# Kernel tuning notes

Hardware: AMD Instinct MI355X
Metric: run time of the kernel (lower is better)

Reference implementation:

```python
import jax, jax.numpy as jnp
import numpy as np

BN_EPS = 1e-5


def setup_inputs() -> dict:
    key = jax.random.key(0)
    ks = jax.random.split(key, 7)
    B, C, N = 8, 512, 2048
    P = C // 2
    x = jax.random.normal(ks[0], (B, C, N), dtype=jnp.float32)
    # 1x1 conv weights (no bias), shape [out, in]
    Wg = jax.random.normal(ks[1], (P, C), dtype=jnp.float32) * (1.0 / np.sqrt(C))
    Wtheta = jax.random.normal(ks[2], (P, C), dtype=jnp.float32) * (1.0 / np.sqrt(C))
    Wphi = jax.random.normal(ks[3], (P, C), dtype=jnp.float32) * (1.0 / np.sqrt(C))
    Wz = jax.random.normal(ks[4], (C, P), dtype=jnp.float32) * (1.0 / np.sqrt(P))
    gamma = jnp.ones((C,), dtype=jnp.float32)
    beta = jnp.zeros((C,), dtype=jnp.float32)
    return {"x": x, "Wg": Wg, "Wtheta": Wtheta, "Wphi": Wphi, "Wz": Wz,
            "gamma": gamma, "beta": beta}


def reference(x, Wg, Wtheta, Wphi, Wz, gamma, beta):
    # x: [B, C, N]
    g = jnp.einsum('pc,bcn->bnp', Wg, x)        # [B, N, P]
    theta = jnp.einsum('pc,bcn->bnp', Wtheta, x)  # [B, N, P]
    phi = jnp.einsum('pc,bcn->bpn', Wphi, x)      # [B, P, N]
    f = jnp.einsum('bnp,bpm->bnm', theta, phi)    # [B, N, N] unscaled scores
    f = jax.nn.softmax(f, axis=-1)
    y = jnp.einsum('bnm,bmp->bpn', f, g)          # [B, P, N]
    z = jnp.einsum('cp,bpn->bcn', Wz, y)          # [B, C, N]
    # BatchNorm1d (training-mode batch stats over batch and length dims)
    mean = jnp.mean(z, axis=(0, 2), keepdims=True)
    var = jnp.mean((z - mean) ** 2, axis=(0, 2), keepdims=True)
    z_bn = (z - mean) / jnp.sqrt(var + BN_EPS)
    z_bn = z_bn * gamma[None, :, None] + beta[None, :, None]
    return z_bn + x
```

## Files before the change

kernel.cpp:

```cpp
#include <hip/hip_runtime.h>
#include <hip/hip_bf16.h>


typedef __attribute__((ext_vector_type(8))) short short8;
typedef __attribute__((ext_vector_type(4))) float floatx4;

__device__ __forceinline__ unsigned short f2bf(float v) {
    __hip_bfloat16 h = __float2bfloat16(v);
    return *(unsigned short*)&h;
}
__device__ __forceinline__ float bf2f(unsigned short u) {
    __hip_bfloat16 h;
    *(unsigned short*)&h = u;
    return __bfloat162float(h);
}

__global__ __launch_bounds__(256) void transpose_split(
    const float* __restrict__ X, unsigned short* __restrict__ Thi,
    unsigned short* __restrict__ Tlo, int R, int N)
{
    X   += (long)blockIdx.z * R * N;
    Thi += (long)blockIdx.z * N * R;
    Tlo += (long)blockIdx.z * N * R;
    __shared__ float s[32][33];
    const int tx = threadIdx.x & 31, ty = threadIdx.x >> 5;
    const int n0 = blockIdx.x * 32, r0 = blockIdx.y * 32;
#pragma unroll
    for (int r = 0; r < 4; ++r)
        s[ty + r * 8][tx] = X[(long)(r0 + ty + r * 8) * N + n0 + tx];
    __syncthreads();
#pragma unroll
    for (int r = 0; r < 4; ++r) {
        const int n = ty + r * 8;
        const float v = s[tx][n];
        const unsigned short hi = f2bf(v);
        const unsigned short lo = f2bf(v - bf2f(hi));
        Thi[(long)(n0 + n) * R + r0 + tx] = hi;
        Tlo[(long)(n0 + n) * R + r0 + tx] = lo;
    }
}

__global__ __launch_bounds__(256) void split_w2(
    const float* __restrict__ Wth, const float* __restrict__ Wph,
    unsigned short* __restrict__ Whi, unsigned short* __restrict__ Wlo, int PC)
{
    const int i = blockIdx.x * 256 + threadIdx.x;
    if (i < 2 * PC) {
        const float v = (i < PC) ? Wth[i] : Wph[i - PC];
        const unsigned short hi = f2bf(v);
        Whi[i] = hi;
        Wlo[i] = f2bf(v - bf2f(hi));
    }
}

__global__ __launch_bounds__(256) void cast_bf16(
    const float* __restrict__ X, unsigned short* __restrict__ Y)
{
    const long i = ((long)blockIdx.x * 256 + threadIdx.x) * 4;
    const float4 v = *(const float4*)&X[i];
    ushort4 o;
    o.x = f2bf(v.x); o.y = f2bf(v.y); o.z = f2bf(v.z); o.w = f2bf(v.w);
    *(ushort4*)&Y[i] = o;
}

#define BK 32

template <bool SPLIT, int OUTMODE, int FM, int FN>
__global__ __launch_bounds__(256) void mfma_gemm(
    const unsigned short* __restrict__ Ahi, const unsigned short* __restrict__ Alo,
    const unsigned short* __restrict__ Bhi, const unsigned short* __restrict__ Blo,
    void* __restrict__ Cout, void* __restrict__ Cout2,
    int K, int lda, int ldb, int ldc,
    long sA, long sB, long sC,
    float* __restrict__ S1, float* __restrict__ S2)
{
    constexpr int MTM = FM * 32, MTN = FN * 32;
    constexpr int SA = FM / 2, SB = FN / 2;

    Ahi += (long)blockIdx.z * sA;
    Bhi += (long)blockIdx.z * sB;
    if (SPLIT) { Alo += (long)blockIdx.z * sA; Blo += (long)blockIdx.z * sB; }
    float* Cf = (float*)Cout + (long)blockIdx.z * sC;
    unsigned short* Ch = (unsigned short*)Cout + (long)blockIdx.z * sC;
    unsigned short* Cl = (unsigned short*)Cout2 + (long)blockIdx.z * sC;

    __shared__ unsigned short AsH[MTM * BK], BsH[MTN * BK];
    __shared__ unsigned short AsL[SPLIT ? MTM * BK : 8], BsL[SPLIT ? MTN * BK : 8];

    const int tid = threadIdx.x;
    const int wid = tid >> 6, lane = tid & 63;
    const int wm = (wid >> 1) * (FM * 16), wn = (wid & 1) * (FN * 16);
    const int l15 = lane & 15, quad = lane >> 4;
    const int m0 = blockIdx.y * MTM, n0 = blockIdx.x * MTN;

    int arow[SA], acol[SA], brow[SB], bcol[SB];
#pragma unroll
    for (int t = 0; t < SA; ++t) {
        const int gid = t * 256 + tid;
        arow[t] = gid >> 2; acol[t] = (gid & 3) * 8;
    }
#pragma unroll
    for (int t = 0; t < SB; ++t) {
        const int gid = t * 256 + tid;
        brow[t] = gid >> 2; bcol[t] = (gid & 3) * 8;
    }

    short8 pa[SA], pb[SB], paL[SPLIT ? SA : 1], pbL[SPLIT ? SB : 1];

    auto loadTiles = [&](int k0) {
#pragma unroll
        for (int t = 0; t < SA; ++t) {
            const long o = (long)(m0 + arow[t]) * lda + k0 + acol[t];
            pa[t] = *(const short8*)&Ahi[o];
            if (SPLIT) paL[t] = *(const short8*)&Alo[o];
        }
#pragma unroll
        for (int t = 0; t < SB; ++t) {
            const long o = (long)(n0 + brow[t]) * ldb + k0 + bcol[t];
            pb[t] = *(const short8*)&Bhi[o];
            if (SPLIT) pbL[t] = *(const short8*)&Blo[o];
        }
    };
    auto writeTiles = [&]() {
#pragma unroll
        for (int t = 0; t < SA; ++t) {
            *(short8*)&AsH[arow[t] * BK + acol[t]] = pa[t];
            if (SPLIT) *(short8*)&AsL[arow[t] * BK + acol[t]] = paL[t];
        }
#pragma unroll
        for (int t = 0; t < SB; ++t) {
            *(short8*)&BsH[brow[t] * BK + bcol[t]] = pb[t];
            if (SPLIT) *(short8*)&BsL[brow[t] * BK + bcol[t]] = pbL[t];
        }
    };

    floatx4 acc[FM][FN];
#pragma unroll
    for (int i = 0; i < FM; ++i)
#pragma unroll
        for (int j = 0; j < FN; ++j) acc[i][j] = (floatx4){0.f, 0.f, 0.f, 0.f};

    const int iters = K / BK;
    loadTiles(0);
    writeTiles();
    __syncthreads();

    for (int it = 0; it < iters; ++it) {
        if (it + 1 < iters) loadTiles((it + 1) * BK);

        short8 ah[FM], bh[FN], al[SPLIT ? FM : 1], bl[SPLIT ? FN : 1];
#pragma unroll
        for (int i = 0; i < FM; ++i) {
            ah[i] = *(const short8*)&AsH[(wm + i * 16 + l15) * BK + quad * 8];
            if (SPLIT) al[i] = *(const short8*)&AsL[(wm + i * 16 + l15) * BK + quad * 8];
        }
#pragma unroll
        for (int j = 0; j < FN; ++j) {
            bh[j] = *(const short8*)&BsH[(wn + j * 16 + l15) * BK + quad * 8];
            if (SPLIT) bl[j] = *(const short8*)&BsL[(wn + j * 16 + l15) * BK + quad * 8];
        }
#pragma unroll
        for (int i = 0; i < FM; ++i)
#pragma unroll
            for (int j = 0; j < FN; ++j) {
                acc[i][j] = __builtin_amdgcn_mfma_f32_16x16x32_bf16(ah[i], bh[j], acc[i][j], 0, 0, 0);
                if (SPLIT) {
                    acc[i][j] = __builtin_amdgcn_mfma_f32_16x16x32_bf16(ah[i], bl[j], acc[i][j], 0, 0, 0);
                    acc[i][j] = __builtin_amdgcn_mfma_f32_16x16x32_bf16(al[i], bh[j], acc[i][j], 0, 0, 0);
                }
            }

        if (it + 1 < iters) {
            __syncthreads();
            writeTiles();
            __syncthreads();
        }
    }

#pragma unroll
    for (int i = 0; i < FM; ++i)
#pragma unroll
        for (int j = 0; j < FN; ++j) {
            const int m = m0 + wm + i * 16 + quad * 4;
            const int n = n0 + wn + j * 16 + l15;
#pragma unroll
            for (int r = 0; r < 4; ++r) {
                const float v = acc[i][j][r];
                const long idx = (long)(m + r) * ldc + n;
                if (OUTMODE == 0) {
                    Cf[idx] = v;
                } else if (OUTMODE == 1 || OUTMODE == 3) {
                    Ch[idx] = f2bf(v);
                } else {
                    const unsigned short hi = f2bf(v);
                    Ch[idx] = hi;
                    Cl[idx] = f2bf(v - bf2f(hi));
                }
            }
        }

    if (OUTMODE == 3) {
        const int slot = (blockIdx.z * gridDim.x + blockIdx.x) * 2 + (wn >> 6);
#pragma unroll
        for (int i = 0; i < FM; ++i)
#pragma unroll
            for (int r = 0; r < 4; ++r) {
                float s = 0.f, q = 0.f;
#pragma unroll
                for (int j = 0; j < FN; ++j) {
                    const float v = acc[i][j][r];
                    s += v; q += v * v;
                }
#pragma unroll
                for (int msk = 1; msk < 16; msk <<= 1) {
                    s += __shfl_xor(s, msk, 64);
                    q += __shfl_xor(q, msk, 64);
                }
                if (l15 == 0) {
                    const int row = m0 + wm + i * 16 + quad * 4 + r;
                    S1[(long)row * 256 + slot] = s;
                    S2[(long)row * 256 + slot] = q;
                }
            }
    }
}

#define PSTRP 136

__device__ __forceinline__ int swz64(int row, int slot) {
    return (row << 6) + (((slot ^ row) & 7) << 3);
}

__global__ __launch_bounds__(256, 2) void fused_attn(
    const unsigned short* __restrict__ thphH,
    const unsigned short* __restrict__ thphL,
    const unsigned short* __restrict__ gbf,
    float* __restrict__ yp,
    float2* __restrict__ ml)
{
    const int N = 2048, P = 256, P2 = 512;
    const int id = blockIdx.x;
    const int b  = id & 7;
    const int kh = (id >> 3) & 3;
    const int qt = id >> 5;
    const int q0 = qt * 64;

    const unsigned short* thB = thphH + (long)b * N * P2;
    const unsigned short* tlB = thphL + (long)b * N * P2;
    const unsigned short* gB  = gbf   + (long)b * P * N;
    float*  ypB = yp + (long)kh * (8L * N * P) + (long)b * N * P;
    float2* mlB = ml + (long)kh * (8L * N) + (long)b * N;

    __shared__ unsigned short FG[2 * 128 * 64];
    unsigned short* Fh = FG;
    unsigned short* Fl = FG + 128 * 64;
    unsigned short* Gs = FG;
    __shared__ unsigned short Pw[4][16 * PSTRP];
    __shared__ float Aly[64];

    const int tid = threadIdx.x;
    const int wid = tid >> 6, lane = tid & 63;
    const int l15 = lane & 15, quad = lane >> 4;

    short8 tHr[8], tLr[8];
    {
        const unsigned short* t1 = thB + (long)(q0 + wid * 16 + l15) * P2;
        const unsigned short* t2 = tlB + (long)(q0 + wid * 16 + l15) * P2;
#pragma unroll
        for (int kt = 0; kt < 8; ++kt) {
            tHr[kt] = *(const short8*)&t1[kt * 32 + quad * 8];
            tLr[kt] = *(const short8*)&t2[kt * 32 + quad * 8];
        }
    }

    float mrun[4], lrun[4];
#pragma unroll
    for (int r = 0; r < 4; ++r) { mrun[r] = -1e30f; lrun[r] = 0.f; }

    floatx4 oacc[16];
#pragma unroll
    for (int p = 0; p < 16; ++p) oacc[p] = (floatx4){0.f, 0.f, 0.f, 0.f};

    const int prow = tid >> 3, slot = tid & 7;
    short8 pfH[4], pfL[4], pg[8];

    auto loadPhi = [&](int m0, int kc) {
#pragma unroll
        for (int s = 0; s < 4; ++s) {
            const long o = (long)(m0 + prow + s * 32) * P2 + P + kc * 64 + slot * 8;
            pfH[s] = *(const short8*)&thB[o];
            pfL[s] = *(const short8*)&tlB[o];
        }
    };
    auto writePhi = [&]() {
#pragma unroll
        for (int s = 0; s < 4; ++s) {
            *(short8*)&Fh[swz64(prow + s * 32, slot)] = pfH[s];
            *(short8*)&Fl[swz64(prow + s * 32, slot)] = pfL[s];
        }
    };
    auto loadG = [&](int m0, int mc) {
#pragma unroll
        for (int s = 0; s < 8; ++s)
            pg[s] = *(const short8*)&gB[(long)(prow + s * 32) * N + m0 + mc * 64 + slot * 8];
    };
    auto writeG = [&]() {
#pragma unroll
        for (int s = 0; s < 8; ++s)
            *(short8*)&Gs[swz64(prow + s * 32, slot)] = pg[s];
    };

    for (int mt = 0; mt < 4; ++mt) {
        const int m0 = kh * 512 + mt * 128;

        floatx4 sacc[8];
#pragma unroll
        for (int j = 0; j < 8; ++j) sacc[j] = (floatx4){0.f, 0.f, 0.f, 0.f};

        loadPhi(m0, 0);
        __syncthreads();
        writePhi();
        __syncthreads();
#pragma unroll
        for (int kc = 0; kc < 4; ++kc) {
            if (kc < 3) loadPhi(m0, kc + 1);
#pragma unroll
            for (int ks = 0; ks < 2; ++ks) {
                const short8 aH = tHr[kc * 2 + ks];
                const short8 aL = tLr[kc * 2 + ks];
#pragma unroll
                for (int j = 0; j < 8; ++j) {
                    const int ro = swz64(j * 16 + l15, ks * 4 + quad);
                    const short8 bh = *(const short8*)&Fh[ro];
                    const short8 bl = *(const short8*)&Fl[ro];
                    sacc[j] = __builtin_amdgcn_mfma_f32_16x16x32_bf16(aH, bh, sacc[j], 0, 0, 0);
                    sacc[j] = __builtin_amdgcn_mfma_f32_16x16x32_bf16(aH, bl, sacc[j], 0, 0, 0);
                    sacc[j] = __builtin_amdgcn_mfma_f32_16x16x32_bf16(aL, bh, sacc[j], 0, 0, 0);
                }
            }
            if (kc < 3) {
                __syncthreads();
                writePhi();
                __syncthreads();
            }
        }

        float alpha[4];
#pragma unroll
        for (int r = 0; r < 4; ++r) {
            float v = sacc[0][r];
#pragma unroll
            for (int j = 1; j < 8; ++j) v = fmaxf(v, sacc[j][r]);
            v = fmaxf(v, __shfl_xor(v, 1, 64));
            v = fmaxf(v, __shfl_xor(v, 2, 64));
            v = fmaxf(v, __shfl_xor(v, 4, 64));
            v = fmaxf(v, __shfl_xor(v, 8, 64));
            const float mo = mrun[r];
            const float mn = fmaxf(mo, v);
            mrun[r] = mn;
            alpha[r] = __expf(mo - mn);
        }
        float lpart[4] = {0.f, 0.f, 0.f, 0.f};
#pragma unroll
        for (int j = 0; j < 8; ++j)
#pragma unroll
            for (int r = 0; r < 4; ++r) {
                const float p = __expf(sacc[j][r] - mrun[r]);
                Pw[wid][(quad * 4 + r) * PSTRP + j * 16 + l15] = f2bf(p);
                lpart[r] += p;
            }
#pragma unroll
        for (int r = 0; r < 4; ++r) {
            float s = lpart[r];
            s += __shfl_xor(s, 1, 64);
            s += __shfl_xor(s, 2, 64);
            s += __shfl_xor(s, 4, 64);
            s += __shfl_xor(s, 8, 64);
            lrun[r] = lrun[r] * alpha[r] + s;
        }
        if (l15 == 0) {
#pragma unroll
            for (int r = 0; r < 4; ++r) Aly[wid * 16 + quad * 4 + r] = alpha[r];
        }

        loadG(m0, 0);
        __syncthreads();
        writeG();
        __syncthreads();

        float alr[4][4];
#pragma unroll
        for (int g = 0; g < 4; ++g)
#pragma unroll
            for (int r = 0; r < 4; ++r) alr[g][r] = Aly[g * 16 + quad * 4 + r];
        int noresc = 1;
#pragma unroll
        for (int g = 0; g < 4; ++g)
#pragma unroll
            for (int r = 0; r < 4; ++r) noresc &= (alr[g][r] == 1.f);
        if (!__all(noresc)) {
#pragma unroll
            for (int g = 0; g < 4; ++g)
#pragma unroll
                for (int pj = 0; pj < 4; ++pj)
#pragma unroll
                    for (int r = 0; r < 4; ++r) oacc[g * 4 + pj][r] *= alr[g][r];
        }

#pragma unroll
        for (int mc = 0; mc < 2; ++mc) {
            if (mc == 0) loadG(m0, 1);
#pragma unroll
            for (int kk = 0; kk < 2; ++kk) {
                short8 af[4];
#pragma unroll
                for (int g = 0; g < 4; ++g)
                    af[g] = *(const short8*)&Pw[g][l15 * PSTRP + mc * 64 + kk * 32 + quad * 8];
#pragma unroll
                for (int pj = 0; pj < 4; ++pj) {
                    const short8 bg = *(const short8*)&Gs[swz64(wid * 64 + pj * 16 + l15, kk * 4 + quad)];
#pragma unroll
                    for (int g = 0; g < 4; ++g)
                        oacc[g * 4 + pj] = __builtin_amdgcn_mfma_f32_16x16x32_bf16(af[g], bg, oacc[g * 4 + pj], 0, 0, 0);
                }
            }
            if (mc == 0) {
                __syncthreads();
                writeG();
                __syncthreads();
            }
        }
    }

    if (l15 == 0) {
#pragma unroll
        for (int r = 0; r < 4; ++r) Aly[wid * 16 + quad * 4 + r] = 1.0f / lrun[r];
    }
    __syncthreads();
    float liv[4][4];
#pragma unroll
    for (int g = 0; g < 4; ++g)
#pragma unroll
        for (int r = 0; r < 4; ++r) liv[g][r] = Aly[g * 16 + quad * 4 + r];
#pragma unroll
    for (int g = 0; g < 4; ++g)
#pragma unroll
        for (int pj = 0; pj < 4; ++pj)
#pragma unroll
            for (int r = 0; r < 4; ++r) {
                const int row = q0 + g * 16 + quad * 4 + r;
                const int col = wid * 64 + pj * 16 + l15;
                ypB[(long)row * P + col] = oacc[g * 4 + pj][r] * liv[g][r];
            }
    if (l15 == 0) {
#pragma unroll
        for (int r = 0; r < 4; ++r) {
            const int row = q0 + wid * 16 + quad * 4 + r;
            mlB[row] = float2{mrun[r], lrun[r]};
        }
    }
}

__global__ __launch_bounds__(256) void attn_merge(
    const float* __restrict__ yp, const float2* __restrict__ ml,
    unsigned short* __restrict__ ybf)
{
    const long STRIDE = 8L * 2048 * 256;
    const long NROWS  = 8L * 2048;
    const long t = (long)blockIdx.x * 256 + threadIdx.x;
    const long row = t >> 5;
    const int  c0  = ((int)t & 31) * 8;
    const float2 a0 = ml[row];
    const float2 a1 = ml[NROWS + row];
    const float2 a2 = ml[2 * NROWS + row];
    const float2 a3 = ml[3 * NROWS + row];
    const float mx = fmaxf(fmaxf(a0.x, a1.x), fmaxf(a2.x, a3.x));
    const float w0 = a0.y * __expf(a0.x - mx);
    const float w1 = a1.y * __expf(a1.x - mx);
    const float w2 = a2.y * __expf(a2.x - mx);
    const float w3 = a3.y * __expf(a3.x - mx);
    const float inv = 1.0f / (w0 + w1 + w2 + w3);
    const float f0 = w0 * inv, f1 = w1 * inv, f2 = w2 * inv, f3 = w3 * inv;
    const long base = row * 256 + c0;
    const float4 u0 = *(const float4*)&yp[base];
    const float4 u1 = *(const float4*)&yp[base + 4];
    const float4 v0 = *(const float4*)&yp[STRIDE + base];
    const float4 v1 = *(const float4*)&yp[STRIDE + base + 4];
    const float4 p0 = *(const float4*)&yp[2 * STRIDE + base];
    const float4 p1 = *(const float4*)&yp[2 * STRIDE + base + 4];
    const float4 q0 = *(const float4*)&yp[3 * STRIDE + base];
    const float4 q1 = *(const float4*)&yp[3 * STRIDE + base + 4];
    ushort4 o0, o1;
    o0.x = f2bf(f0 * u0.x + f1 * v0.x + f2 * p0.x + f3 * q0.x);
    o0.y = f2bf(f0 * u0.y + f1 * v0.y + f2 * p0.y + f3 * q0.y);
    o0.z = f2bf(f0 * u0.z + f1 * v0.z + f2 * p0.z + f3 * q0.z);
    o0.w = f2bf(f0 * u0.w + f1 * v0.w + f2 * p0.w + f3 * q0.w);
    o1.x = f2bf(f0 * u1.x + f1 * v1.x + f2 * p1.x + f3 * q1.x);
    o1.y = f2bf(f0 * u1.y + f1 * v1.y + f2 * p1.y + f3 * q1.y);
    o1.z = f2bf(f0 * u1.z + f1 * v1.z + f2 * p1.z + f3 * q1.z);
    o1.w = f2bf(f0 * u1.w + f1 * v1.w + f2 * p1.w + f3 * q1.w);
    *(ushort4*)&ybf[base] = o0;
    *(ushort4*)&ybf[base + 4] = o1;
}

__global__ __launch_bounds__(256) void bn_finalize(
    const float* __restrict__ p1, const float* __restrict__ p2,
    float* __restrict__ mean, float* __restrict__ rstd, float cnt)
{
    const int c = blockIdx.x, t = threadIdx.x;
    __shared__ float rs[256], rq[256];
    rs[t] = p1[(long)c * 256 + t];
    rq[t] = p2[(long)c * 256 + t];
    __syncthreads();
    for (int st = 128; st > 0; st >>= 1) {
        if (t < st) { rs[t] += rs[t + st]; rq[t] += rq[t + st]; }
        __syncthreads();
    }
    if (t == 0) {
        const float m = rs[0] / cnt;
        mean[c] = m;
        rstd[c] = rsqrtf(rq[0] / cnt - m * m + 1e-5f);
    }
}

__global__ __launch_bounds__(256) void bn_apply_bf(
    const unsigned short* __restrict__ z, const float* __restrict__ x,
    const float* __restrict__ mean, const float* __restrict__ rstd,
    const float* __restrict__ gamma, const float* __restrict__ beta,
    float* __restrict__ out, int C, int N)
{
    const long i = ((long)blockIdx.x * 256 + threadIdx.x) * 8;
    const int c = (int)((i / N) % C);
    const float mu = mean[c], rs = rstd[c], ga = gamma[c], be = beta[c];
    const ushort4 z0 = *(const ushort4*)&z[i];
    const ushort4 z1 = *(const ushort4*)&z[i + 4];
    const float4 x0 = *(const float4*)&x[i];
    const float4 x1 = *(const float4*)&x[i + 4];
    float4 o0, o1;
    o0.x = (bf2f(z0.x) - mu) * rs * ga + be + x0.x;
    o0.y = (bf2f(z0.y) - mu) * rs * ga + be + x0.y;
    o0.z = (bf2f(z0.z) - mu) * rs * ga + be + x0.z;
    o0.w = (bf2f(z0.w) - mu) * rs * ga + be + x0.w;
    o1.x = (bf2f(z1.x) - mu) * rs * ga + be + x1.x;
    o1.y = (bf2f(z1.y) - mu) * rs * ga + be + x1.y;
    o1.z = (bf2f(z1.z) - mu) * rs * ga + be + x1.z;
    o1.w = (bf2f(z1.w) - mu) * rs * ga + be + x1.w;
    *(float4*)&out[i] = o0;
    *(float4*)&out[i + 4] = o1;
}

extern "C" void kernel_launch(void* const* d_in, const int* in_sizes, int n_in,
                              void* d_out, int out_size, void* d_ws, size_t ws_size,
                              hipStream_t stream)
{
    const int B = 8, C = 512, N = 2048, P = 256;
    const float* x      = (const float*)d_in[0];
    const float* Wg     = (const float*)d_in[1];
    const float* Wtheta = (const float*)d_in[2];
    const float* Wphi   = (const float*)d_in[3];
    const float* Wz     = (const float*)d_in[4];
    const float* gamma  = (const float*)d_in[5];
    const float* beta   = (const float*)d_in[6];
    float* out = (float*)d_out;

    float* ws = (float*)d_ws;
    const long NCle = (long)N * C;
    const long NP   = (long)N * P;
    const long R0   = (long)B * NCle;
    unsigned short* xtH   = (unsigned short*)ws;
    unsigned short* xtL   = xtH + B * NCle;
    unsigned short* zbf   = (unsigned short*)ws;
    unsigned short* thphH = (unsigned short*)(ws + R0);
    unsigned short* thphL = thphH + B * NCle;
    unsigned short* gbf   = (unsigned short*)(ws + 2 * R0);
    unsigned short* fbf   = gbf + B * NP;
    unsigned short* ybf   = fbf + (long)B * N * N;
    unsigned short* W2H   = ybf + B * NP;
    unsigned short* W2L   = W2H + 2L * P * C;
    unsigned short* WgB   = W2L + 2L * P * C;
    unsigned short* WzB   = WgB + (long)P * C;
    float*          yp    = (float*)fbf;
    float2*         ml    = (float2*)(ws + 6L * 1024 * 1024);
    float*          bnp1  = ws + R0;
    float*          bnp2  = bnp1 + (long)C * 256;
    float*          mean  = bnp2 + (long)C * 256;
    float*          rstd  = mean + C;

    const long sX = (long)C * N;
    const int  P2 = 2 * P;

    transpose_split<<<dim3(N / 32, C / 32, B), 256, 0, stream>>>(x, xtH, xtL, C, N);
    split_w2<<<(2 * P * C + 255) / 256, 256, 0, stream>>>(Wtheta, Wphi, W2H, W2L, P * C);
    cast_bf16<<<P * C / 1024, 256, 0, stream>>>(Wg, WgB);
    cast_bf16<<<P * C / 1024, 256, 0, stream>>>(Wz, WzB);

    mfma_gemm<true, 2, 4, 4><<<dim3(P2 / 128, N / 128, B), 256, 0, stream>>>(
        xtH, xtL, W2H, W2L, thphH, thphL, C, C, C, P2, NCle, 0, NCle, nullptr, nullptr);
    mfma_gemm<false, 1, 2, 4><<<dim3(N / 128, P / 64, B), 256, 0, stream>>>(
        WgB, WgB, xtH, xtH, gbf, gbf, C, C, C, N, 0, NCle, NP, nullptr, nullptr);

    fused_attn<<<dim3(1024), 256, 0, stream>>>(thphH, thphL, gbf, yp, ml);
    attn_merge<<<dim3(2048), 256, 0, stream>>>(yp, ml, ybf);

    mfma_gemm<false, 3, 4, 4><<<dim3(N / 128, C / 128, B), 256, 0, stream>>>(
        WzB, WzB, ybf, ybf, zbf, zbf, P, P, P, N, 0, NP, sX, bnp1, bnp2);

    bn_finalize<<<C, 256, 0, stream>>>(bnp1, bnp2, mean, rstd, (float)B * N);
    bn_apply_bf<<<(int)((B * sX) / 2048), 256, 0, stream>>>(zbf, x, mean, rstd, gamma, beta, out, C, N);
}
```

Baseline: 288.3 us.

## Double-buffer phi and g LDS tiles with one barrier per step and MFMA priority

Splits the 64-wide LDS chunks for phi and g into two 32-wide halves used as a ping-pong buffer. The kernel then prefetches two steps ahead and writes the next half while the current half is consumed, which cuts synchronisation from two barriers per chunk to one. It also raises wave priority around the MFMA bursts with s_setprio. The cost is more loop iterations with smaller K steps, and correctness now depends on the half-buffer indexing being race-free.

Result: faster. 281.7 us (-2.3%).

```diff
diff --git a/kernel.cpp b/kernel.cpp
--- a/kernel.cpp
+++ b/kernel.cpp
@@ -281,34 +281,9 @@
 #pragma unroll
     for (int p = 0; p < 16; ++p) oacc[p] = (floatx4){0.f, 0.f, 0.f, 0.f};
 
-    const int prow = tid >> 3, slot = tid & 7;
-    short8 pfH[4], pfL[4], pg[8];
-
-    auto loadPhi = [&](int m0, int kc) {
-#pragma unroll
-        for (int s = 0; s < 4; ++s) {
-            const long o = (long)(m0 + prow + s * 32) * P2 + P + kc * 64 + slot * 8;
-            pfH[s] = *(const short8*)&thB[o];
-            pfL[s] = *(const short8*)&tlB[o];
-        }
-    };
-    auto writePhi = [&]() {
-#pragma unroll
-        for (int s = 0; s < 4; ++s) {
-            *(short8*)&Fh[swz64(prow + s * 32, slot)] = pfH[s];
-            *(short8*)&Fl[swz64(prow + s * 32, slot)] = pfL[s];
-        }
-    };
-    auto loadG = [&](int m0, int mc) {
-#pragma unroll
-        for (int s = 0; s < 8; ++s)
-            pg[s] = *(const short8*)&gB[(long)(prow + s * 32) * N + m0 + mc * 64 + slot * 8];
-    };
-    auto writeG = [&]() {
-#pragma unroll
-        for (int s = 0; s < 8; ++s)
-            *(short8*)&Gs[swz64(prow + s * 32, slot)] = pg[s];
-    };
+    const int prow4 = tid >> 2, lslot = tid & 3;
+    short8 pfH[2][2], pfL[2][2];
+    short8 pg[2][4];
 
     for (int mt = 0; mt < 4; ++mt) {
         const int m0 = kh * 512 + mt * 128;
@@ -317,32 +292,60 @@
 #pragma unroll
         for (int j = 0; j < 8; ++j) sacc[j] = (floatx4){0.f, 0.f, 0.f, 0.f};
 
-        loadPhi(m0, 0);
+#pragma unroll
+        for (int s = 0; s < 2; ++s) {
+            const long o = (long)(m0 + s * 64 + prow4) * P2 + P + 0 * 32 + lslot * 8;
+            pfH[0][s] = *(const short8*)&thB[o];
+            pfL[0][s] = *(const short8*)&tlB[o];
+        }
+#pragma unroll
+        for (int s = 0; s < 2; ++s) {
+            const int row = s * 64 + prow4;
+            *(short8*)&Fh[swz64(row, lslot)] = pfH[0][s];
+            *(short8*)&Fl[swz64(row, lslot)] = pfL[0][s];
+        }
+#pragma unroll
+        for (int s = 0; s < 2; ++s) {
+            const long o = (long)(m0 + s * 64 + prow4) * P2 + P + 1 * 32 + lslot * 8;
+            pfH[1][s] = *(const short8*)&thB[o];
+            pfL[1][s] = *(const short8*)&tlB[o];
+        }
         __syncthreads();
-        writePhi();
-        __syncthreads();
-#pragma unroll
-        for (int kc = 0; kc < 4; ++kc) {
-            if (kc < 3) loadPhi(m0, kc + 1);
-#pragma unroll
-            for (int ks = 0; ks < 2; ++ks) {
-                const short8 aH = tHr[kc * 2 + ks];
-                const short8 aL = tLr[kc * 2 + ks];
-#pragma unroll
-                for (int j = 0; j < 8; ++j) {
-                    const int ro = swz64(j * 16 + l15, ks * 4 + quad);
-                    const short8 bh = *(const short8*)&Fh[ro];
-                    const short8 bl = *(const short8*)&Fl[ro];
-                    sacc[j] = __builtin_amdgcn_mfma_f32_16x16x32_bf16(aH, bh, sacc[j], 0, 0, 0);
-                    sacc[j] = __builtin_amdgcn_mfma_f32_16x16x32_bf16(aH, bl, sacc[j], 0, 0, 0);
-                    sacc[j] = __builtin_amdgcn_mfma_f32_16x16x32_bf16(aL, bh, sacc[j], 0, 0, 0);
+
+#pragma unroll
+        for (int kc = 0; kc < 8; ++kc) {
+            if (kc < 6) {
+#pragma unroll
+                for (int s = 0; s < 2; ++s) {
+                    const long o = (long)(m0 + s * 64 + prow4) * P2 + P + (kc + 2) * 32 + lslot * 8;
+                    pfH[kc & 1][s] = *(const short8*)&thB[o];
+                    pfL[kc & 1][s] = *(const short8*)&tlB[o];
                 }
             }
-            if (kc < 3) {
-                __syncthreads();
-                writePhi();
-                __syncthreads();
-            }
+            const short8 aH = tHr[kc];
+            const short8 aL = tLr[kc];
+            const int half = (kc & 1) * 4;
+            __builtin_amdgcn_s_setprio(1);
+#pragma unroll
+            for (int j = 0; j < 8; ++j) {
+                const int ro = swz64(j * 16 + l15, half + quad);
+                const short8 bh = *(const short8*)&Fh[ro];
+                const short8 bl = *(const short8*)&Fl[ro];
+                sacc[j] = __builtin_amdgcn_mfma_f32_16x16x32_bf16(aH, bh, sacc[j], 0, 0, 0);
+                sacc[j] = __builtin_amdgcn_mfma_f32_16x16x32_bf16(aH, bl, sacc[j], 0, 0, 0);
+                sacc[j] = __builtin_amdgcn_mfma_f32_16x16x32_bf16(aL, bh, sacc[j], 0, 0, 0);
+            }
+            __builtin_amdgcn_s_setprio(0);
+            if (kc < 7) {
+                const int wh = ((kc + 1) & 1) * 4;
+#pragma unroll
+                for (int s = 0; s < 2; ++s) {
+                    const int row = s * 64 + prow4;
+                    *(short8*)&Fh[swz64(row, wh + lslot)] = pfH[(kc + 1) & 1][s];
+                    *(short8*)&Fl[swz64(row, wh + lslot)] = pfL[(kc + 1) & 1][s];
+                }
+            }
+            __syncthreads();
         }
 
         float alpha[4];
@@ -383,9 +386,15 @@
             for (int r = 0; r < 4; ++r) Aly[wid * 16 + quad * 4 + r] = alpha[r];
         }
 
-        loadG(m0, 0);
-        __syncthreads();
-        writeG();
+#pragma unroll
+        for (int s = 0; s < 4; ++s)
+            pg[0][s] = *(const short8*)&gB[(long)(s * 64 + prow4) * N + m0 + 0 * 32 + lslot * 8];
+#pragma unroll
+        for (int s = 0; s < 4; ++s)
+            *(short8*)&Gs[swz64(s * 64 + prow4, lslot)] = pg[0][s];
+#pragma unroll
+        for (int s = 0; s < 4; ++s)
+            pg[1][s] = *(const short8*)&gB[(long)(s * 64 + prow4) * N + m0 + 1 * 32 + lslot * 8];
         __syncthreads();
 
         float alr[4][4];
@@ -408,25 +417,31 @@
         }
 
 #pragma unroll
-        for (int mc = 0; mc < 2; ++mc) {
-            if (mc == 0) loadG(m0, 1);
-#pragma unroll
-            for (int kk = 0; kk < 2; ++kk) {
-                short8 af[4];
+        for (int mc = 0; mc < 4; ++mc) {
+            if (mc < 2) {
+#pragma unroll
+                for (int s = 0; s < 4; ++s)
+                    pg[mc & 1][s] = *(const short8*)&gB[(long)(s * 64 + prow4) * N + m0 + (mc + 2) * 32 + lslot * 8];
+            }
+            const int half = (mc & 1) * 4;
+            short8 af[4];
+#pragma unroll
+            for (int g = 0; g < 4; ++g)
+                af[g] = *(const short8*)&Pw[g][l15 * PSTRP + mc * 32 + quad * 8];
+            __builtin_amdgcn_s_setprio(1);
+#pragma unroll
+            for (int pj = 0; pj < 4; ++pj) {
+                const short8 bg = *(const short8*)&Gs[swz64(wid * 64 + pj * 16 + l15, half + quad)];
 #pragma unroll
                 for (int g = 0; g < 4; ++g)
-                    af[g] = *(const short8*)&Pw[g][l15 * PSTRP + mc * 64 + kk * 32 + quad * 8];
-#pragma unroll
-                for (int pj = 0; pj < 4; ++pj) {
-                    const short8 bg = *(const short8*)&Gs[swz64(wid * 64 + pj * 16 + l15, kk * 4 + quad)];
-#pragma unroll
-                    for (int g = 0; g < 4; ++g)
-                        oacc[g * 4 + pj] = __builtin_amdgcn_mfma_f32_16x16x32_bf16(af[g], bg, oacc[g * 4 + pj], 0, 0, 0);
-                }
-            }
-            if (mc == 0) {
-                __syncthreads();
-                writeG();
+                    oacc[g * 4 + pj] = __builtin_amdgcn_mfma_f32_16x16x32_bf16(af[g], bg, oacc[g * 4 + pj], 0, 0, 0);
+            }
+            __builtin_amdgcn_s_setprio(0);
+            if (mc < 3) {
+                const int wh = ((mc + 1) & 1) * 4;
+#pragma unroll
+                for (int s = 0; s < 4; ++s)
+                    *(short8*)&Gs[swz64(s * 64 + prow4, wh + lslot)] = pg[(mc + 1) & 1][s];
                 __syncthreads();
             }
         }
```
